# Kernel tuning notes

Hardware: AMD Instinct MI355X
Metric: run time of the kernel (lower is better)

The kernel has to match this reference:

```python
import jax, jax.numpy as jnp
import numpy as np

B, S, ENC, DEC, ATT = 32, 2048, 1024, 1024, 1024


def setup_inputs() -> dict:
    key = jax.random.key(0)
    k1, k2, k3, k4, k5 = jax.random.split(key, 5)
    return {
        "keys": jax.random.normal(k1, (B, S, ENC), dtype=jnp.float32),
        "q": jax.random.normal(k2, (B, DEC), dtype=jnp.float32),
        "W_e2a": jax.random.normal(k3, (ATT, ENC), dtype=jnp.float32),
        "W_d2a": jax.random.normal(k4, (ATT, DEC), dtype=jnp.float32),
        "v_w": jax.random.normal(k5, (ATT, 1), dtype=jnp.float32),
    }


def reference(keys, q, W_e2a, W_d2a, v_w):
    # U: [B, S, ATT] = keys @ W_e2a.T
    U = jnp.einsum("bse,ae->bsa", keys, W_e2a)
    # V: [B, ATT] broadcast over S
    V = jnp.einsum("bd,ad->ba", q, W_d2a)
    # scores e: [B, S]
    e = jnp.einsum("bsa,a->bs", jnp.tanh(U + V[:, None, :]), v_w[:, 0])
    a = jax.nn.softmax(e, axis=1)
    # context: [B, ENC]
    context = jnp.einsum("bs,bse->be", a, keys)
    return context
```

## Files before the change

kernel.cpp:

```cpp
#include <hip/hip_runtime.h>
#include <stdint.h>

#define NB 32
#define NS 2048
#define NE 1024
#define ND 1024
#define NA 1024
#define MROWS (NB * NS)

typedef float f32x4 __attribute__((ext_vector_type(4)));
typedef int i32x4 __attribute__((ext_vector_type(4)));

typedef __attribute__((address_space(3))) unsigned int lds_u32;
typedef __attribute__((address_space(1))) unsigned int glb_u32;

__device__ __forceinline__ float tanh_fast(float x){
  float ax = fabsf(x);
  float e = __expf(-2.0f * ax);
  float t = (1.0f - e) * __builtin_amdgcn_rcpf(1.0f + e);
  return x < 0.0f ? -t : t;
}
__device__ __forceinline__ void gload_lds16(const void* g, void* l){
  __builtin_amdgcn_global_load_lds((const glb_u32*)g, (lds_u32*)l, 16, 0, 0);
}

#define VMCNT0()  asm volatile("s_waitcnt vmcnt(0)" ::: "memory")

__global__ __launch_bounds__(256) void quant_kernel(
    const float* __restrict__ src, unsigned char* __restrict__ dh,
    unsigned char* __restrict__ dl, float* __restrict__ sdst)
{
  const int t = threadIdx.x;
  const int w = t >> 6, l = t & 63;
  const int row = blockIdx.x * 4 + w;
  const float* sp = src + (size_t)row * 1024;

  f32x4 x[4];
  #pragma unroll
  for (int c = 0; c < 4; ++c)
    x[c] = *reinterpret_cast<const f32x4*>(sp + c * 256 + l * 4);

  float m = 0.0f;
  #pragma unroll
  for (int c = 0; c < 4; ++c)
    #pragma unroll
    for (int j = 0; j < 4; ++j) m = fmaxf(m, fabsf(x[c][j]));
  #pragma unroll
  for (int off = 1; off < 64; off <<= 1) m = fmaxf(m, __shfl_xor(m, off, 64));
  m = fmaxf(m, 1e-30f);
  const float s = m * (1.0f / 126.0f);
  const float inv = 126.0f / m;

  const int r = row & 255;
  const int rp = r >> 1, cc = r & 1;
  const int kb = (l >> 2) & 3;
  const int gran = (cc << 2) | (kb ^ (rp & 3));
  const size_t base = ((size_t)(row >> 8) << 18) + ((size_t)rp << 7)
                    + ((size_t)gran << 4) + ((l & 3) << 2);

  #pragma unroll
  for (int c = 0; c < 4; ++c){
    int hw = 0, lw = 0;
    #pragma unroll
    for (int j = 0; j < 4; ++j){
      float f = x[c][j] * inv;
      float hf = rintf(f);
      float lf = fminf(rintf((f - hf) * 256.0f), 127.0f);
      hw |= (((int)hf) & 255) << (8 * j);
      lw |= (((int)lf) & 255) << (8 * j);
    }
    const int g = c * 4 + (l >> 4);
    *reinterpret_cast<int*>(dh + base + ((size_t)g << 14)) = hw;
    *reinterpret_cast<int*>(dl + base + ((size_t)g << 14)) = lw;
  }
  if (l == 0) sdst[row] = s;
}

__global__ __launch_bounds__(256) void v_kernel(
    const float* __restrict__ q, const float* __restrict__ Wd,
    float* __restrict__ V)
{
  int gw = blockIdx.x * 4 + (threadIdx.x >> 6);
  int l = threadIdx.x & 63;
  int b = gw >> 10, a = gw & 1023;
  const float* qp = q + b * ND;
  const float* wp = Wd + (size_t)a * ND;
  float s = 0.0f;
  #pragma unroll
  for (int c = 0; c < 4; ++c){
    int off = c * 256 + l * 4;
    f32x4 q4 = *reinterpret_cast<const f32x4*>(qp + off);
    f32x4 w4 = *reinterpret_cast<const f32x4*>(wp + off);
    s += q4[0]*w4[0] + q4[1]*w4[1] + q4[2]*w4[2] + q4[3]*w4[3];
  }
  #pragma unroll
  for (int off = 1; off < 64; off <<= 1) s += __shfl_xor(s, off, 64);
  if (l == 0) V[gw] = s;
}

__global__ __launch_bounds__(256, 2) void score_i8_kernel(
    const unsigned char* __restrict__ Kq_h,
    const unsigned char* __restrict__ Kq_l,
    const unsigned char* __restrict__ Wq_h,
    const unsigned char* __restrict__ Wq_l,
    const float* __restrict__ sA, const float* __restrict__ sB,
    const float* __restrict__ Vb, const float* __restrict__ vw,
    float* __restrict__ e_part)
{
  __shared__ __align__(16) unsigned char shb[65536];
  __shared__ float ebuf[2][128];
  __shared__ float sAl[128];
  __shared__ float sBl[128];

  const int t = threadIdx.x;
  const int w = t >> 6, l = t & 63;
  const int l15 = l & 15, lg = l >> 4;
  const int wr = w >> 1, wc = w & 1;

  const int orig = blockIdx.x;
  const int xcd = orig & 7;
  const int s0 = orig >> 3;
  const int nchunk = s0 & 7;
  const int mtile = ((s0 >> 3) << 3) | xcd;
  const int row0 = mtile << 7;
  const int nb0 = nchunk << 7;
  const int bb = row0 >> 11;

  const size_t aoff_src = ((size_t)(mtile >> 1) << 18)
                        + ((size_t)(mtile & 1) << 13) + ((size_t)wr << 12);
  const unsigned char* Asrc_h = Kq_h + aoff_src;
  const unsigned char* Asrc_l = Kq_l + aoff_src;
  const size_t boff_src = ((size_t)(nchunk >> 1) << 18) + ((size_t)(nchunk & 1) << 13);

  const int swzg = ((((l15 & 1) << 2) | (lg ^ ((l15 >> 1) & 3)))) << 4;
  const int aloc0 = ((l15 >> 1) << 7) + swzg;
  const int boff0 = (wc << 12) + ((l15 >> 1) << 7) + swzg;
  const int stl = l << 4;

  const int wbase = w << 14;

  const unsigned char* pBh = Wq_h + boff_src + boff0;
  const unsigned char* pBl = Wq_l + boff_src + boff0;

  i32x4 acc1[4][4], acc2[4][4];
  #pragma unroll
  for (int mf = 0; mf < 4; ++mf)
    #pragma unroll
    for (int nf = 0; nf < 4; ++nf){ acc1[mf][nf] = (i32x4)0; acc2[mf][nf] = (i32x4)0; }

  auto stageA = [&](int g, int buf){
    const size_t gb = (size_t)g << 14;
    unsigned char* d = shb + wbase + (buf << 13);
    #pragma unroll
    for (int i = 0; i < 4; ++i){
      gload_lds16(Asrc_h + gb + (i << 10) + stl, d + (i << 10) + stl);
      gload_lds16(Asrc_l + gb + (i << 10) + stl, d + 4096 + (i << 10) + stl);
    }
  };

  i32x4 BhA[4], BhB[4];

  #pragma unroll
  for (int nf = 0; nf < 4; ++nf)
    BhA[nf] = *reinterpret_cast<const i32x4*>(pBh + nf * 1024);
  stageA(0, 0);
  if (t < 128){ sAl[t] = sA[row0 + t]; sBl[t] = sB[nb0 + t]; }
  __syncthreads();

  auto body = [&](int g, i32x4 (&Bhcur)[4], i32x4 (&Bhnext)[4]){
    VMCNT0();
    const int buf = g & 1;
    const unsigned char* base = shb + wbase + (buf << 13);

    if (g < 15){
      const size_t gb1 = (size_t)(g + 1) << 14;
      #pragma unroll
      for (int nf = 0; nf < 4; ++nf)
        Bhnext[nf] = *reinterpret_cast<const i32x4*>(pBh + gb1 + nf * 1024);
      stageA(g + 1, buf ^ 1);
    }
    i32x4 Bl[4];
    {
      const size_t gb = (size_t)g << 14;
      #pragma unroll
      for (int nf = 0; nf < 4; ++nf)
        Bl[nf] = *reinterpret_cast<const i32x4*>(pBl + gb + nf * 1024);
    }

    i32x4 Ah[4];
    #pragma unroll
    for (int mf = 0; mf < 4; ++mf)
      Ah[mf] = *reinterpret_cast<const i32x4*>(base + aloc0 + mf * 1024);
    __builtin_amdgcn_s_setprio(1);
    #pragma unroll
    for (int nf = 0; nf < 4; ++nf)
      #pragma unroll
      for (int mf = 0; mf < 4; ++mf)
        acc1[mf][nf] = __builtin_amdgcn_mfma_i32_16x16x64_i8(Ah[mf], Bhcur[nf], acc1[mf][nf], 0, 0, 0);
    __builtin_amdgcn_s_setprio(0);

    i32x4 Al[4];
    #pragma unroll
    for (int mf = 0; mf < 4; ++mf)
      Al[mf] = *reinterpret_cast<const i32x4*>(base + 4096 + aloc0 + mf * 1024);
    __builtin_amdgcn_s_setprio(1);
    #pragma unroll
    for (int nf = 0; nf < 4; ++nf)
      #pragma unroll
      for (int mf = 0; mf < 4; ++mf)
        acc2[mf][nf] = __builtin_amdgcn_mfma_i32_16x16x64_i8(Al[mf], Bhcur[nf], acc2[mf][nf], 0, 0, 0);
    __builtin_amdgcn_s_setprio(0);

    __builtin_amdgcn_s_setprio(1);
    #pragma unroll
    for (int nf = 0; nf < 4; ++nf)
      #pragma unroll
      for (int mf = 0; mf < 4; ++mf)
        acc2[mf][nf] = __builtin_amdgcn_mfma_i32_16x16x64_i8(Ah[mf], Bl[nf], acc2[mf][nf], 0, 0, 0);
    __builtin_amdgcn_s_setprio(0);
  };

  #pragma unroll 1
  for (int gp = 0; gp < 8; ++gp){
    body(2 * gp,     BhA, BhB);
    body(2 * gp + 1, BhB, BhA);
  }

  float sav[16];
  #pragma unroll
  for (int mf = 0; mf < 4; ++mf)
    #pragma unroll
    for (int i = 0; i < 4; ++i)
      sav[(mf << 2) + i] = sAl[(wr << 6) + (mf << 4) + (lg << 2) + i];

  float er[16];
  #pragma unroll
  for (int j = 0; j < 16; ++j) er[j] = 0.0f;
  #pragma unroll
  for (int nf = 0; nf < 4; ++nf){
    const int nl = (wc << 6) + (nf << 4) + l15;
    const int n = nb0 + nl;
    const float sb = sBl[nl];
    const float Vl = Vb[bb * NA + n];
    const float vwl = vw[n];
    #pragma unroll
    for (int mf = 0; mf < 4; ++mf)
      #pragma unroll
      for (int i = 0; i < 4; ++i){
        float U = sav[(mf << 2) + i] * sb *
                  ((float)acc1[mf][nf][i] + (float)acc2[mf][nf][i] * 0.00390625f);
        er[(mf << 2) + i] += tanh_fast(U + Vl) * vwl;
      }
  }
  #pragma unroll
  for (int j = 0; j < 16; ++j){
    #pragma unroll
    for (int off = 1; off < 16; off <<= 1)
      er[j] += __shfl_xor(er[j], off, 64);
  }
  if (l15 == 0){
    #pragma unroll
    for (int mf = 0; mf < 4; ++mf)
      #pragma unroll
      for (int i = 0; i < 4; ++i)
        ebuf[wc][(wr << 6) + (mf << 4) + (lg << 2) + i] = er[(mf << 2) + i];
  }
  __syncthreads();
  if (t < 128)
    e_part[(size_t)nchunk * MROWS + row0 + t] = ebuf[0][t] + ebuf[1][t];
}

__global__ __launch_bounds__(256) void softmax_kernel(
    const float* __restrict__ e_part, float* __restrict__ a)
{
  __shared__ float red[4];
  const int b = blockIdx.x;
  const int t = threadIdx.x;
  const int l = t & 63, w = t >> 6;
  const float* ep = e_part + b * NS + t * 8;
  float v[8];
  #pragma unroll
  for (int j = 0; j < 8; ++j) v[j] = 0.0f;
  #pragma unroll
  for (int c = 0; c < 8; ++c){
    f32x4 x0 = *reinterpret_cast<const f32x4*>(ep + (size_t)c * MROWS);
    f32x4 x1 = *reinterpret_cast<const f32x4*>(ep + (size_t)c * MROWS + 4);
    #pragma unroll
    for (int j = 0; j < 4; ++j){ v[j] += x0[j]; v[4 + j] += x1[j]; }
  }

  float m = v[0];
  #pragma unroll
  for (int j = 1; j < 8; ++j) m = fmaxf(m, v[j]);
  #pragma unroll
  for (int off = 1; off < 64; off <<= 1) m = fmaxf(m, __shfl_xor(m, off, 64));
  if (l == 0) red[w] = m;
  __syncthreads();
  m = fmaxf(fmaxf(red[0], red[1]), fmaxf(red[2], red[3]));
  __syncthreads();

  float ex[8];
  float ssum = 0.0f;
  #pragma unroll
  for (int j = 0; j < 8; ++j){ ex[j] = __expf(v[j] - m); ssum += ex[j]; }
  #pragma unroll
  for (int off = 1; off < 64; off <<= 1) ssum += __shfl_xor(ssum, off, 64);
  if (l == 0) red[w] = ssum;
  __syncthreads();
  ssum = red[0] + red[1] + red[2] + red[3];
  float inv = 1.0f / ssum;

  float o[8];
  #pragma unroll
  for (int j = 0; j < 8; ++j) o[j] = ex[j] * inv;
  float* ap = a + b * NS + t * 8;
  *reinterpret_cast<f32x4*>(ap)     = *reinterpret_cast<f32x4*>(&o[0]);
  *reinterpret_cast<f32x4*>(ap + 4) = *reinterpret_cast<f32x4*>(&o[4]);
}

__global__ __launch_bounds__(256) void ctx_partial_i8_kernel(
    const float* __restrict__ a, const unsigned char* __restrict__ Kq_h,
    const unsigned char* __restrict__ Kq_l, const float* __restrict__ sA,
    float* __restrict__ part)
{
  const int bid = blockIdx.x;
  const int t = threadIdx.x;
  const int g = t >> 4;
  const int kb = (t >> 2) & 3;
  const size_t ibase = ((size_t)bid << 18) + ((size_t)g << 14) + ((size_t)(t & 3) << 2);
  const float* ap = a + bid * 256;
  const float* sp = sA + bid * 256;
  f32x4 accv = (f32x4)0.0f;
  for (int si = 0; si < 256; ++si){
    const int rp = si >> 1, cc = si & 1;
    const size_t addr = ibase + ((size_t)rp << 7)
                      + ((size_t)(((cc << 2) | (kb ^ (rp & 3))) << 4));
    const int h32 = *reinterpret_cast<const int*>(Kq_h + addr);
    const int l32 = *reinterpret_cast<const int*>(Kq_l + addr);
    const float sa = sp[si];
    const float t1 = ap[si] * sa;
    const float t2 = t1 * 0.00390625f;
    #pragma unroll
    for (int j = 0; j < 4; ++j){
      int hj = (h32 << ((3 - j) * 8)) >> 24;
      int lj = (l32 << ((3 - j) * 8)) >> 24;
      accv[j] += t1 * (float)hj + t2 * (float)lj;
    }
  }
  *reinterpret_cast<f32x4*>(part + (size_t)bid * NE + t * 4) = accv;
}

__global__ __launch_bounds__(256) void ctx_reduce_kernel(
    const float* __restrict__ part, float* __restrict__ out)
{
  const int b = blockIdx.x;
  const int t = threadIdx.x;
  f32x4 s = (f32x4)0.0f;
  #pragma unroll
  for (int sc = 0; sc < 8; ++sc)
    s += *reinterpret_cast<const f32x4*>(part + (size_t)((b << 3) + sc) * NE + t * 4);
  *reinterpret_cast<f32x4*>(out + b * NE + t * 4) = s;
}

extern "C" void kernel_launch(void* const* d_in, const int* in_sizes, int n_in,
                              void* d_out, int out_size, void* d_ws, size_t ws_size,
                              hipStream_t stream)
{
  const float* keys = (const float*)d_in[0];
  const float* q    = (const float*)d_in[1];
  const float* We   = (const float*)d_in[2];
  const float* Wd   = (const float*)d_in[3];
  const float* vw   = (const float*)d_in[4];
  float* out = (float*)d_out;

  char* ws = (char*)d_ws;
  const size_t MB = 1024 * 1024;
  unsigned char* Wq_h = (unsigned char*)(ws);
  unsigned char* Wq_l = (unsigned char*)(ws + 1 * MB);
  float* sB     = (float*)(ws + 2 * MB);
  float* sA     = (float*)(ws + 2 * MB + 65536);
  float* Vb     = (float*)(ws + 2 * MB + 393216);
  float* e_part = (float*)(ws + 4 * MB);
  float* a      = (float*)(ws + 6 * MB);
  unsigned char* Kq_h = (unsigned char*)(ws + 8 * MB);
  unsigned char* Kq_l = (unsigned char*)(ws + 72 * MB);
  float* part   = e_part;

  quant_kernel<<<256,   256, 0, stream>>>(We,   Wq_h, Wq_l, sB);
  quant_kernel<<<16384, 256, 0, stream>>>(keys, Kq_h, Kq_l, sA);
  v_kernel<<<(NB * NA) / 4, 256, 0, stream>>>(q, Wd, Vb);
  score_i8_kernel<<<4096, 256, 0, stream>>>(Kq_h, Kq_l, Wq_h, Wq_l,
                                            sA, sB, Vb, vw, e_part);
  softmax_kernel<<<NB, 256, 0, stream>>>(e_part, a);
  ctx_partial_i8_kernel<<<NB * 8, 256, 0, stream>>>(a, Kq_h, Kq_l, sA, part);
  ctx_reduce_kernel<<<NB, 256, 0, stream>>>(part, out);
}
```

Measured before the change: 333.8 us.

## Stagger K-loop start per block and hoist LDS A loads before prefetch

Odd-numbered blocks now start the K-group loop at group 8 and wrap around, so neighbouring blocks read different parts of the weights and keys at the same time. Both the high and low A fragments are now read from LDS at the top of each iteration, before the next stage's global-to-LDS prefetch is issued. The s_setprio priority bumps around the MFMA blocks are removed. The aim is to spread memory traffic across channels and to separate LDS reads from the incoming writes, at the cost of more live registers and different wave scheduling.

New measurement: 342.5 us. +2.6%, slower.

```diff
diff --git a/kernel.cpp b/kernel.cpp
--- a/kernel.cpp
+++ b/kernel.cpp
@@ -126,6 +126,8 @@
   const int nb0 = nchunk << 7;
   const int bb = row0 >> 11;
 
+  const int g0 = (orig & 1) << 3;
+
   const size_t aoff_src = ((size_t)(mtile >> 1) << 18)
                         + ((size_t)(mtile & 1) << 13) + ((size_t)wr << 12);
   const unsigned char* Asrc_h = Kq_h + aoff_src;
@@ -162,22 +164,31 @@
 
   #pragma unroll
   for (int nf = 0; nf < 4; ++nf)
-    BhA[nf] = *reinterpret_cast<const i32x4*>(pBh + nf * 1024);
-  stageA(0, 0);
+    BhA[nf] = *reinterpret_cast<const i32x4*>(pBh + ((size_t)g0 << 14) + nf * 1024);
+  stageA(g0, 0);
   if (t < 128){ sAl[t] = sA[row0 + t]; sBl[t] = sB[nb0 + t]; }
   __syncthreads();
 
-  auto body = [&](int g, i32x4 (&Bhcur)[4], i32x4 (&Bhnext)[4]){
+  auto body = [&](int i, i32x4 (&Bhcur)[4], i32x4 (&Bhnext)[4]){
     VMCNT0();
-    const int buf = g & 1;
+    const int g = (g0 + i) & 15;
+    const int buf = i & 1;
     const unsigned char* base = shb + wbase + (buf << 13);
 
-    if (g < 15){
-      const size_t gb1 = (size_t)(g + 1) << 14;
+    i32x4 Ah[4], Al[4];
+    #pragma unroll
+    for (int mf = 0; mf < 4; ++mf){
+      Ah[mf] = *reinterpret_cast<const i32x4*>(base + aloc0 + mf * 1024);
+      Al[mf] = *reinterpret_cast<const i32x4*>(base + 4096 + aloc0 + mf * 1024);
+    }
+
+    if (i < 15){
+      const int gn = (g0 + i + 1) & 15;
+      const size_t gb1 = (size_t)gn << 14;
       #pragma unroll
       for (int nf = 0; nf < 4; ++nf)
         Bhnext[nf] = *reinterpret_cast<const i32x4*>(pBh + gb1 + nf * 1024);
-      stageA(g + 1, buf ^ 1);
+      stageA(gn, buf ^ 1);
     }
     i32x4 Bl[4];
     {
@@ -187,43 +198,29 @@
         Bl[nf] = *reinterpret_cast<const i32x4*>(pBl + gb + nf * 1024);
     }
 
-    i32x4 Ah[4];
-    #pragma unroll
-    for (int mf = 0; mf < 4; ++mf)
-      Ah[mf] = *reinterpret_cast<const i32x4*>(base + aloc0 + mf * 1024);
-    __builtin_amdgcn_s_setprio(1);
     #pragma unroll
     for (int nf = 0; nf < 4; ++nf)
       #pragma unroll
       for (int mf = 0; mf < 4; ++mf)
         acc1[mf][nf] = __builtin_amdgcn_mfma_i32_16x16x64_i8(Ah[mf], Bhcur[nf], acc1[mf][nf], 0, 0, 0);
-    __builtin_amdgcn_s_setprio(0);
-
-    i32x4 Al[4];
-    #pragma unroll
-    for (int mf = 0; mf < 4; ++mf)
-      Al[mf] = *reinterpret_cast<const i32x4*>(base + 4096 + aloc0 + mf * 1024);
-    __builtin_amdgcn_s_setprio(1);
+
     #pragma unroll
     for (int nf = 0; nf < 4; ++nf)
       #pragma unroll
       for (int mf = 0; mf < 4; ++mf)
         acc2[mf][nf] = __builtin_amdgcn_mfma_i32_16x16x64_i8(Al[mf], Bhcur[nf], acc2[mf][nf], 0, 0, 0);
-    __builtin_amdgcn_s_setprio(0);
-
-    __builtin_amdgcn_s_setprio(1);
+
     #pragma unroll
     for (int nf = 0; nf < 4; ++nf)
       #pragma unroll
       for (int mf = 0; mf < 4; ++mf)
         acc2[mf][nf] = __builtin_amdgcn_mfma_i32_16x16x64_i8(Ah[mf], Bl[nf], acc2[mf][nf], 0, 0, 0);
-    __builtin_amdgcn_s_setprio(0);
   };
 
   #pragma unroll 1
-  for (int gp = 0; gp < 8; ++gp){
-    body(2 * gp,     BhA, BhB);
-    body(2 * gp + 1, BhB, BhA);
+  for (int ip = 0; ip < 8; ++ip){
+    body(2 * ip,     BhA, BhB);
+    body(2 * ip + 1, BhB, BhA);
   }
 
   float sav[16];
```

## Restructure score kernel to 8 waves sharing one LDS A tile per block

Applied to the files above, without the earlier changes.

The score GEMM block grows from 4 to 8 waves (2x4 wave grid), each wave now computing a 64x32 subtile instead of 64x64. The A tile is staged once per block into a shared 32KB LDS double buffer instead of a private per-wave region, with a block-wide barrier each K step. B register double-buffering is dropped in favor of direct per-step loads. The intent is to cut LDS footprint and raise occupancy and A reuse, at the cost of per-step barriers and less latency hiding for B loads.

Result: no change. 329.4 us (-1.3%).

```diff
diff --git a/kernel.cpp b/kernel.cpp
--- a/kernel.cpp
+++ b/kernel.cpp
@@ -98,7 +98,7 @@
   if (l == 0) V[gw] = s;
 }
 
-__global__ __launch_bounds__(256, 2) void score_i8_kernel(
+__global__ __launch_bounds__(512, 4) void score_i8_kernel(
     const unsigned char* __restrict__ Kq_h,
     const unsigned char* __restrict__ Kq_l,
     const unsigned char* __restrict__ Wq_h,
@@ -107,15 +107,16 @@
     const float* __restrict__ Vb, const float* __restrict__ vw,
     float* __restrict__ e_part)
 {
-  __shared__ __align__(16) unsigned char shb[65536];
-  __shared__ float ebuf[2][128];
+  __shared__ __align__(16) unsigned char shb[32768];
+  __shared__ float ebuf[4][128];
   __shared__ float sAl[128];
   __shared__ float sBl[128];
 
   const int t = threadIdx.x;
   const int w = t >> 6, l = t & 63;
   const int l15 = l & 15, lg = l >> 4;
-  const int wr = w >> 1, wc = w & 1;
+  const int wr = w >> 2;
+  const int wc2 = w & 3;
 
   const int orig = blockIdx.x;
   const int xcd = orig & 7;
@@ -126,104 +127,86 @@
   const int nb0 = nchunk << 7;
   const int bb = row0 >> 11;
 
-  const size_t aoff_src = ((size_t)(mtile >> 1) << 18)
-                        + ((size_t)(mtile & 1) << 13) + ((size_t)wr << 12);
+  const size_t aoff_src = ((size_t)(mtile >> 1) << 18) + ((size_t)(mtile & 1) << 13);
   const unsigned char* Asrc_h = Kq_h + aoff_src;
   const unsigned char* Asrc_l = Kq_l + aoff_src;
   const size_t boff_src = ((size_t)(nchunk >> 1) << 18) + ((size_t)(nchunk & 1) << 13);
 
   const int swzg = ((((l15 & 1) << 2) | (lg ^ ((l15 >> 1) & 3)))) << 4;
-  const int aloc0 = ((l15 >> 1) << 7) + swzg;
-  const int boff0 = (wc << 12) + ((l15 >> 1) << 7) + swzg;
-  const int stl = l << 4;
-
-  const int wbase = w << 14;
-
-  const unsigned char* pBh = Wq_h + boff_src + boff0;
-  const unsigned char* pBl = Wq_l + boff_src + boff0;
-
-  i32x4 acc1[4][4], acc2[4][4];
+  const int aloc0 = (wr << 12) + ((l15 >> 1) << 7) + swzg;
+  const int bloc0 = (wc2 << 11) + ((l15 >> 1) << 7) + swzg;
+  const int stl = t << 4;
+
+  const unsigned char* pBh = Wq_h + boff_src + bloc0;
+  const unsigned char* pBl = Wq_l + boff_src + bloc0;
+
+  i32x4 acc1[4][2], acc2[4][2];
   #pragma unroll
   for (int mf = 0; mf < 4; ++mf)
     #pragma unroll
-    for (int nf = 0; nf < 4; ++nf){ acc1[mf][nf] = (i32x4)0; acc2[mf][nf] = (i32x4)0; }
+    for (int nf = 0; nf < 2; ++nf){ acc1[mf][nf] = (i32x4)0; acc2[mf][nf] = (i32x4)0; }
 
   auto stageA = [&](int g, int buf){
     const size_t gb = (size_t)g << 14;
-    unsigned char* d = shb + wbase + (buf << 13);
-    #pragma unroll
-    for (int i = 0; i < 4; ++i){
-      gload_lds16(Asrc_h + gb + (i << 10) + stl, d + (i << 10) + stl);
-      gload_lds16(Asrc_l + gb + (i << 10) + stl, d + 4096 + (i << 10) + stl);
-    }
+    unsigned char* d = shb + (buf << 14);
+    gload_lds16(Asrc_h + gb + stl, d + stl);
+    gload_lds16(Asrc_l + gb + stl, d + 8192 + stl);
   };
 
-  i32x4 BhA[4], BhB[4];
-
-  #pragma unroll
-  for (int nf = 0; nf < 4; ++nf)
-    BhA[nf] = *reinterpret_cast<const i32x4*>(pBh + nf * 1024);
   stageA(0, 0);
   if (t < 128){ sAl[t] = sA[row0 + t]; sBl[t] = sB[nb0 + t]; }
-  __syncthreads();
-
-  auto body = [&](int g, i32x4 (&Bhcur)[4], i32x4 (&Bhnext)[4]){
-    VMCNT0();
+  VMCNT0();
+  __syncthreads();
+
+  #pragma unroll 1
+  for (int g = 0; g < 16; ++g){
     const int buf = g & 1;
-    const unsigned char* base = shb + wbase + (buf << 13);
-
-    if (g < 15){
-      const size_t gb1 = (size_t)(g + 1) << 14;
-      #pragma unroll
-      for (int nf = 0; nf < 4; ++nf)
-        Bhnext[nf] = *reinterpret_cast<const i32x4*>(pBh + gb1 + nf * 1024);
-      stageA(g + 1, buf ^ 1);
+    const unsigned char* base = shb + (buf << 14);
+
+    i32x4 Ah[4], Al[4];
+    #pragma unroll
+    for (int mf = 0; mf < 4; ++mf){
+      Ah[mf] = *reinterpret_cast<const i32x4*>(base + aloc0 + mf * 1024);
+      Al[mf] = *reinterpret_cast<const i32x4*>(base + 8192 + aloc0 + mf * 1024);
     }
-    i32x4 Bl[4];
+    if (g < 15) stageA(g + 1, buf ^ 1);
+    i32x4 Bh[2], Bl[2];
     {
       const size_t gb = (size_t)g << 14;
       #pragma unroll
-      for (int nf = 0; nf < 4; ++nf)
+      for (int nf = 0; nf < 2; ++nf){
+        Bh[nf] = *reinterpret_cast<const i32x4*>(pBh + gb + nf * 1024);
         Bl[nf] = *reinterpret_cast<const i32x4*>(pBl + gb + nf * 1024);
+      }
     }
 
-    i32x4 Ah[4];
-    #pragma unroll
-    for (int mf = 0; mf < 4; ++mf)
-      Ah[mf] = *reinterpret_cast<const i32x4*>(base + aloc0 + mf * 1024);
     __builtin_amdgcn_s_setprio(1);
     #pragma unroll
-    for (int nf = 0; nf < 4; ++nf)
+    for (int nf = 0; nf < 2; ++nf)
       #pragma unroll
       for (int mf = 0; mf < 4; ++mf)
-        acc1[mf][nf] = __builtin_amdgcn_mfma_i32_16x16x64_i8(Ah[mf], Bhcur[nf], acc1[mf][nf], 0, 0, 0);
+        acc1[mf][nf] = __builtin_amdgcn_mfma_i32_16x16x64_i8(Ah[mf], Bh[nf], acc1[mf][nf], 0, 0, 0);
     __builtin_amdgcn_s_setprio(0);
 
-    i32x4 Al[4];
-    #pragma unroll
-    for (int mf = 0; mf < 4; ++mf)
-      Al[mf] = *reinterpret_cast<const i32x4*>(base + 4096 + aloc0 + mf * 1024);
     __builtin_amdgcn_s_setprio(1);
     #pragma unroll
-    for (int nf = 0; nf < 4; ++nf)
+    for (int nf = 0; nf < 2; ++nf)
       #pragma unroll
       for (int mf = 0; mf < 4; ++mf)
-        acc2[mf][nf] = __builtin_amdgcn_mfma_i32_16x16x64_i8(Al[mf], Bhcur[nf], acc2[mf][nf], 0, 0, 0);
+        acc2[mf][nf] = __builtin_amdgcn_mfma_i32_16x16x64_i8(Al[mf], Bh[nf], acc2[mf][nf], 0, 0, 0);
     __builtin_amdgcn_s_setprio(0);
 
     __builtin_amdgcn_s_setprio(1);
     #pragma unroll
-    for (int nf = 0; nf < 4; ++nf)
+    for (int nf = 0; nf < 2; ++nf)
       #pragma unroll
       for (int mf = 0; mf < 4; ++mf)
         acc2[mf][nf] = __builtin_amdgcn_mfma_i32_16x16x64_i8(Ah[mf], Bl[nf], acc2[mf][nf], 0, 0, 0);
     __builtin_amdgcn_s_setprio(0);
-  };
-
-  #pragma unroll 1
-  for (int gp = 0; gp < 8; ++gp){
-    body(2 * gp,     BhA, BhB);
-    body(2 * gp + 1, BhB, BhA);
+
+    VMCNT0();
+    BARRIER_DUMMY:;
+    __builtin_amdgcn_s_barrier();
   }
 
   float sav[16];
@@ -237,8 +220,8 @@
   #pragma unroll
   for (int j = 0; j < 16; ++j) er[j] = 0.0f;
   #pragma unroll
-  for (int nf = 0; nf < 4; ++nf){
-    const int nl = (wc << 6) + (nf << 4) + l15;
+  for (int nf = 0; nf < 2; ++nf){
+    const int nl = (wc2 << 5) + (nf << 4) + l15;
     const int n = nb0 + nl;
     const float sb = sBl[nl];
     const float Vl = Vb[bb * NA + n];
@@ -263,11 +246,12 @@
     for (int mf = 0; mf < 4; ++mf)
       #pragma unroll
       for (int i = 0; i < 4; ++i)
-        ebuf[wc][(wr << 6) + (mf << 4) + (lg << 2) + i] = er[(mf << 2) + i];
+        ebuf[wc2][(wr << 6) + (mf << 4) + (lg << 2) + i] = er[(mf << 2) + i];
   }
   __syncthreads();
   if (t < 128)
-    e_part[(size_t)nchunk * MROWS + row0 + t] = ebuf[0][t] + ebuf[1][t];
+    e_part[(size_t)nchunk * MROWS + row0 + t] =
+        ebuf[0][t] + ebuf[1][t] + ebuf[2][t] + ebuf[3][t];
 }
 
 __global__ __launch_bounds__(256) void softmax_kernel(
@@ -389,7 +373,7 @@
   quant_kernel<<<256,   256, 0, stream>>>(We,   Wq_h, Wq_l, sB);
   quant_kernel<<<16384, 256, 0, stream>>>(keys, Kq_h, Kq_l, sA);
   v_kernel<<<(NB * NA) / 4, 256, 0, stream>>>(q, Wd, Vb);
-  score_i8_kernel<<<4096, 256, 0, stream>>>(Kq_h, Kq_l, Wq_h, Wq_l,
+  score_i8_kernel<<<4096, 512, 0, stream>>>(Kq_h, Kq_l, Wq_h, Wq_l,
                                             sA, sB, Vb, vw, e_part);
   softmax_kernel<<<NB, 256, 0, stream>>>(e_part, a);
   ctx_partial_i8_kernel<<<NB * 8, 256, 0, stream>>>(a, Kq_h, Kq_l, sA, part);
```
